# Optimization experiments

Hardware: AMD Instinct MI355X
Metric: run time of the kernel (lower is better)

Reference implementation:

```python
import jax, jax.numpy as jnp
import numpy as np

COMMITMENT_COST = 0.25


def setup_inputs() -> dict:
    key = jax.random.key(0)
    k1, k2 = jax.random.split(key)
    z = jax.random.normal(k1, (8, 256, 64, 64), dtype=jnp.float32)
    # codebook initialized uniform(-1/K, 1/K) in the original; scale a normal sample similarly
    K, D = 4096, 256
    codebook = jax.random.uniform(k2, (K, D), dtype=jnp.float32, minval=-1.0 / K, maxval=1.0 / K)
    return {"z": z, "codebook": codebook}


def reference(z, codebook):
    # z: [B, C, H, W] -> [B, H, W, C]
    B, C, H, W = z.shape
    K, D = codebook.shape  # D == C
    inputs = jnp.transpose(z, (0, 2, 3, 1))          # [B,H,W,D]
    flat = inputs.reshape(-1, D)                     # [N,D]

    d = (jnp.sum(flat ** 2, axis=1, keepdims=True)
         + jnp.sum(codebook ** 2, axis=1)
         - 2.0 * flat @ codebook.T)
    idx = jnp.argmin(d, axis=1)                      # [N]
    encodings = jax.nn.one_hot(idx, K, dtype=flat.dtype)  # [N,K]
    quantized = (encodings @ codebook).reshape(inputs.shape)  # [B,H,W,D]

    e_latent_loss = jnp.mean((jax.lax.stop_gradient(quantized) - inputs) ** 2)
    q_latent_loss = jnp.mean((quantized - jax.lax.stop_gradient(inputs)) ** 2)
    loss = q_latent_loss + COMMITMENT_COST * e_latent_loss

    # straight-through estimator
    quantized = inputs + jax.lax.stop_gradient(quantized - inputs)

    avg_probs = jnp.mean(encodings, axis=0)          # [K]
    perplexity = jnp.exp(-jnp.sum(avg_probs * jnp.log(avg_probs + 1e-10)))

    quantized_out = jnp.transpose(quantized, (0, 3, 1, 2))  # [B,C,H,W]
    return loss, quantized_out, perplexity, encodings, idx[:, None]
```

## Files before the change

### kernel.cpp

```cpp
#include <hip/hip_runtime.h>
#include <math.h>

#define N_ROWS 32768
#define K_CODES 4096
#define D_DIM 256
#define HW 4096
#define CHW 1048576

#define OFF_LOSS  0
#define OFF_QUANT 1ULL
#define OFF_PERP  8388609ULL
#define OFF_ENC   8388610ULL
#define OFF_IDX   142606338ULL

#define WS_RN   0
#define WS_EN   32768
#define WS_KEY  36864
#define WS_CNT  102400
#define WS_LOSS 106496
#define WS_CCNT 106498
#define WS_CNT2 106499
#define WS_THR  106504
#define WS_CAND 139272
#define CAP     1048576
#define WS_CBF  1187848
#define WS_NEED_BYTES ((1187848ULL + 524288ULL) * 4ULL)

#define MARGIN 1.5e-3f
#define LBUF_N 1536
#define CBUF_N 640

typedef short bf16x8 __attribute__((ext_vector_type(8)));
typedef float f32x4 __attribute__((ext_vector_type(4)));
typedef float f32x2 __attribute__((ext_vector_type(2)));

__device__ __forceinline__ unsigned short f2bf(float f) {
  unsigned u = __float_as_uint(f);
  unsigned r = u + 0x7FFFu + ((u >> 16) & 1u);
  return (unsigned short)(r >> 16);
}

__device__ __forceinline__ void async16(void* lds, const void* g) {
  typedef const __attribute__((address_space(1))) void* gvp;
  typedef __attribute__((address_space(3))) void* lvp;
  __builtin_amdgcn_global_load_lds((gvp)g, (lvp)lds, 16, 0, 0);
}

__device__ __forceinline__ float pairwise_sq_128(const float* __restrict__ p, int stride) {
  float r[8];
#pragma unroll
  for (int j = 0; j < 8; ++j) { float v = p[(size_t)j * stride]; r[j] = v * v; }
#pragma unroll
  for (int g = 1; g < 16; ++g) {
#pragma unroll
    for (int j = 0; j < 8; ++j) { float v = p[(size_t)(g * 8 + j) * stride]; r[j] += v * v; }
  }
  return ((r[0] + r[1]) + (r[2] + r[3])) + ((r[4] + r[5]) + (r[6] + r[7]));
}

__global__ void rownorm_k(const float* __restrict__ z, float* __restrict__ rn) {
  int row = blockIdx.x * 256 + threadIdx.x;
  const float* p = z + (size_t)(row >> 12) * CHW + (row & (HW - 1));
  rn[row] = pairwise_sq_128(p, HW) + pairwise_sq_128(p + (size_t)128 * HW, HW);
}

__global__ void enorm_k(const float* __restrict__ cb, float* __restrict__ en) {
  int k = blockIdx.x * 256 + threadIdx.x;
  const float* p = cb + (size_t)k * D_DIM;
  en[k] = pairwise_sq_128(p, 1) + pairwise_sq_128(p + 128, 1);
}

__global__ void cbbf_k(const float* __restrict__ cb, unsigned short* __restrict__ cbf) {
  int i = (blockIdx.x * 256 + threadIdx.x) * 4;
  float4 v = *(const float4*)(cb + i);
  unsigned d0 = f2bf(v.x) | ((unsigned)f2bf(v.y) << 16);
  unsigned d1 = f2bf(v.z) | ((unsigned)f2bf(v.w) << 16);
  *(int2*)(cbf + i) = make_int2((int)d0, (int)d1);
}

__device__ __forceinline__ void stageB(const unsigned short* __restrict__ cbf,
                                       short* bs, int tile, int ph2, int tid) {
#pragma unroll
  for (int k = 0; k < 4; ++k) {
    int i = tid + k * 256;
    int ks2 = i >> 9, s = i & 511;
    int ct = s >> 6, g = (s >> 4) & 3, m = s & 15;
    const unsigned short* src =
        cbf + (size_t)(tile * 128 + ct * 16 + m) * 256 + ph2 * 64 + ks2 * 32 + g * 8;
    async16(bs + (size_t)i * 8, src);
  }
}

__global__ __launch_bounds__(256, 2) void pass5v_k(
    const float* __restrict__ z, const float* __restrict__ cb,
    const unsigned short* __restrict__ cbf,
    const float* __restrict__ en, float* __restrict__ rn,
    float* __restrict__ enc, unsigned long long* __restrict__ key,
    unsigned int* __restrict__ cand, unsigned int* __restrict__ cnt2) {
  __shared__ __align__(16) short ASw[4 * 8 * 64 * 8];
  __shared__ __align__(16) short BS2[2 * 1024 * 8];
  __shared__ unsigned int lbuf[2 * LBUF_N];
  __shared__ unsigned int cbuf[CBUF_N];
  __shared__ float rmf[64];
  __shared__ float rn_s[64];
  __shared__ unsigned int lcnt, ccnt;

  const int tid = threadIdx.x;
  const int lane = tid & 63;
  const int w = tid >> 6;
  const int row_base = blockIdx.x * 64;
  const float* zb = z + (size_t)(row_base >> 12) * CHW + (row_base & (HW - 1));

  if (tid == 0) { lcnt = 0; ccnt = 0; }

  {
    float* pf = (float*)BS2;
    int f4 = tid & 15;
    int r0 = f4 * 4;
    int g16 = tid >> 4;
#pragma unroll
    for (int it = 0; it < 2; ++it) {
      int c_oct = (tid >> 4) + it * 16;
      float4 v[8];
#pragma unroll
      for (int j = 0; j < 8; ++j)
        v[j] = *(const float4*)(zb + (size_t)(c_oct * 8 + j) * HW + r0);
      int s = c_oct >> 2, g = c_oct & 3;
#pragma unroll
      for (int i = 0; i < 4; ++i) {
        int r = r0 + i, rt = r >> 4, m = r & 15;
        int dw[4];
#pragma unroll
        for (int k = 0; k < 4; ++k) {
          unsigned lo = f2bf(((const float*)&v[2 * k])[i]);
          unsigned hi = f2bf(((const float*)&v[2 * k + 1])[i]);
          dw[k] = (int)(lo | (hi << 16));
        }
        *(int4*)&ASw[(((rt * 8 + s) * 64) + g * 16 + m) * 8] =
            make_int4(dw[0], dw[1], dw[2], dw[3]);
#pragma unroll
        for (int j = 0; j < 8; ++j) {
          float x = ((const float*)&v[j])[i];
          pf[(g16 * 64 + r) * 8 + j] = x * x;
        }
      }
      __syncthreads();
      if (tid < 64) {
        float racc[8];
#pragma unroll
        for (int j = 0; j < 8; ++j) racc[j] = pf[(size_t)tid * 8 + j];
        for (int gg = 1; gg < 16; ++gg)
#pragma unroll
          for (int j = 0; j < 8; ++j) racc[j] += pf[(gg * 64 + tid) * 8 + j];
        float h = ((racc[0] + racc[1]) + (racc[2] + racc[3])) +
                  ((racc[4] + racc[5]) + (racc[6] + racc[7]));
        if (it == 0) rmf[tid] = h;
        else {
          float tot = rmf[tid] + h;
          rn[row_base + tid] = tot;
          rn_s[tid] = tot;
        }
      }
      __syncthreads();
    }
  }

  unsigned rowenc[4];
#pragma unroll
  for (int r = 0; r < 4; ++r)
    rowenc[r] = (unsigned)(row_base + w * 16 + (lane >> 4) * 4 + r) << 12;

  float rmin[4] = {3.4e38f, 3.4e38f, 3.4e38f, 3.4e38f};

  stageB(cbf, BS2, 0, 0, tid);
  int pidx = 0;
  for (int tile = 0; tile < 32; ++tile) {
    float ev[8];
#pragma unroll
    for (int ct = 0; ct < 8; ++ct) ev[ct] = en[tile * 128 + ct * 16 + (lane & 15)];

    f32x4 acc[8];
#pragma unroll
    for (int ct = 0; ct < 8; ++ct) acc[ct] = (f32x4){0.f, 0.f, 0.f, 0.f};

#pragma unroll
    for (int ph2 = 0; ph2 < 4; ++ph2, ++pidx) {
      __syncthreads();
      int nx = pidx + 1;
      if (nx < 128) stageB(cbf, BS2 + (nx & 1) * 8192, nx >> 2, nx & 3, tid);

      const short* bb = BS2 + (pidx & 1) * 8192;
      bf16x8 a0 = *(const bf16x8*)&ASw[((w * 8 + ph2 * 2 + 0) * 64 + lane) * 8];
      bf16x8 a1 = *(const bf16x8*)&ASw[((w * 8 + ph2 * 2 + 1) * 64 + lane) * 8];
      __builtin_amdgcn_s_setprio(1);
#pragma unroll
      for (int ct = 0; ct < 8; ++ct) {
        bf16x8 b0 = *(const bf16x8*)&bb[(ct * 64 + lane) * 8];
        acc[ct] = __builtin_amdgcn_mfma_f32_16x16x32_bf16(a0, b0, acc[ct], 0, 0, 0);
      }
#pragma unroll
      for (int ct = 0; ct < 8; ++ct) {
        bf16x8 b1 = *(const bf16x8*)&bb[(512 + ct * 64 + lane) * 8];
        acc[ct] = __builtin_amdgcn_mfma_f32_16x16x32_bf16(a1, b1, acc[ct], 0, 0, 0);
      }
      __builtin_amdgcn_s_setprio(0);
    }

    {
      f32x2 zz = (f32x2){0.f, 0.f};
      f32x2* dst = (f32x2*)enc + ((size_t)blockIdx.x * 32 + tile) * 4096 + tid;
#pragma unroll
      for (int k = 0; k < 16; ++k)
        __builtin_nontemporal_store(zz, dst + k * 256);
    }

#pragma unroll
    for (int ct = 0; ct < 8; ++ct)
#pragma unroll
      for (int r = 0; r < 4; ++r)
        rmin[r] = fminf(rmin[r], ev[ct] - 2.0f * acc[ct][r]);

    float thr2[4];
#pragma unroll
    for (int r = 0; r < 4; ++r) {
      float v = rmin[r];
      v = fminf(v, __shfl_xor(v, 1));
      v = fminf(v, __shfl_xor(v, 2));
      v = fminf(v, __shfl_xor(v, 4));
      v = fminf(v, __shfl_xor(v, 8));
      thr2[r] = v + MARGIN;
    }

#pragma unroll
    for (int ct = 0; ct < 8; ++ct) {
      unsigned code = (unsigned)(tile * 128 + ct * 16 + (lane & 15));
#pragma unroll
      for (int r = 0; r < 4; ++r) {
        float s = ev[ct] - 2.0f * acc[ct][r];
        if (s <= thr2[r]) {
          unsigned pc = rowenc[r] | code;
          unsigned pos = atomicAdd(&lcnt, 1u);
          if (pos < LBUF_N) {
            lbuf[2 * pos] = pc;
            lbuf[2 * pos + 1] = __float_as_uint(s);
          } else {
            unsigned g = atomicAdd(cnt2, 1u);
            if (g < CAP) cand[g] = pc;
          }
        }
      }
    }
  }

#pragma unroll
  for (int r = 0; r < 4; ++r) {
    float v = rmin[r];
    v = fminf(v, __shfl_xor(v, 1));
    v = fminf(v, __shfl_xor(v, 2));
    v = fminf(v, __shfl_xor(v, 4));
    v = fminf(v, __shfl_xor(v, 8));
    if ((lane & 15) == 0) rmf[(rowenc[r] >> 12) & 63] = v;
  }

  __syncthreads();
  unsigned n = lcnt; if (n > LBUF_N) n = LBUF_N;
  for (unsigned i0 = 0; i0 < n; i0 += 256) {
    unsigned i = i0 + tid;
    bool keep = false; unsigned pc = 0;
    if (i < n) {
      pc = lbuf[2 * i];
      float s = __uint_as_float(lbuf[2 * i + 1]);
      keep = (s <= rmf[(pc >> 12) & 63] + MARGIN);
    }
    unsigned long long m = __ballot(keep);
    unsigned wb = 0;
    if ((tid & 63) == 0 && m) wb = atomicAdd(&ccnt, (unsigned)__popcll(m));
    wb = __shfl(wb, 0);
    if (keep) {
      unsigned off = (unsigned)__popcll(m & ((1ull << (tid & 63)) - 1ull));
      unsigned g = wb + off;
      if (g < CBUF_N) cbuf[g] = pc;
      else { unsigned gg = atomicAdd(cnt2, 1u); if (gg < CAP) cand[gg] = pc; }
    }
  }

  __syncthreads();
  unsigned nv = ccnt; if (nv > CBUF_N) nv = CBUF_N;
  for (unsigned i = tid; i < nv; i += 256) {
    unsigned pc = cbuf[i];
    unsigned row = pc >> 12, code = pc & 4095u;
    const float* x = z + (size_t)(row >> 12) * CHW + (row & (HW - 1));
    const float* e = cb + (size_t)code * D_DIM;
    float acc = 0.0f;
#pragma unroll 8
    for (int c = 0; c < D_DIM; ++c) acc = fmaf(x[(size_t)c * HW], e[c], acc);
    float d = (rn_s[row & 63] + en[code]) - 2.0f * acc;
    unsigned long long k64 = ((unsigned long long)__float_as_uint(d) << 32) | code;
    atomicMin(&key[row], k64);
  }
}

__global__ void verify_k(const float* __restrict__ z, const float* __restrict__ cb,
                         const float* __restrict__ rn, const float* __restrict__ en,
                         const unsigned int* __restrict__ cand,
                         const unsigned int* __restrict__ cnt,
                         unsigned long long* __restrict__ key) {
  unsigned total = *cnt; if (total > CAP) total = CAP;
  for (unsigned i = blockIdx.x * 256 + threadIdx.x; i < total; i += gridDim.x * 256) {
    unsigned pc = cand[i];
    unsigned row = pc >> 12, code = pc & 4095u;
    const float* x = z + (size_t)(row >> 12) * CHW + (row & (HW - 1));
    const float* e = cb + (size_t)code * D_DIM;
    float acc = 0.0f;
#pragma unroll 8
    for (int c = 0; c < D_DIM; ++c) acc = fmaf(x[(size_t)c * HW], e[c], acc);
    float d = (rn[row] + en[code]) - 2.0f * acc;
    unsigned long long k64 = ((unsigned long long)__float_as_uint(d) << 32) | code;
    atomicMin(&key[row], k64);
  }
}

#define BM 128
#define BN 128
#define BK 32
#define KQ 1024
#define ES_S 36
__global__ __launch_bounds__(256, 3) void argmin_fb(
    const float* __restrict__ z, const float* __restrict__ cb,
    const float* __restrict__ rn, const float* __restrict__ en,
    unsigned long long* __restrict__ key, const unsigned int* __restrict__ guard) {
  if (guard && *guard <= CAP) return;
  __shared__ union {
    struct { float Xs[BK * BM]; float Es[BN * ES_S]; } s;
    struct { float rv[BM * 16]; int ri[BM * 16]; } r;
  } sh;
  const int tid = threadIdx.x;
  const int tx = tid & 15, ty = tid >> 4;
  const int row_base = (blockIdx.x >> 2) * BM;
  const int q = blockIdx.x & 3;
  const float* zb = z + (size_t)(row_base >> 12) * CHW + (row_base & (HW - 1));
  float rnv[8];
#pragma unroll
  for (int i = 0; i < 8; ++i) rnv[i] = rn[row_base + ty * 8 + i];
  float bestV[8]; int bestI[8];
#pragma unroll
  for (int i = 0; i < 8; ++i) { bestV[i] = 3.4e38f; bestI[i] = 0; }
  for (int t0 = q * KQ; t0 < q * KQ + KQ; t0 += BN) {
    float acc[8][8];
#pragma unroll
    for (int i = 0; i < 8; ++i)
#pragma unroll
      for (int j = 0; j < 8; ++j) acc[i][j] = 0.0f;
    for (int kb = 0; kb < D_DIM; kb += BK) {
      __syncthreads();
#pragma unroll
      for (int k = 0; k < 4; ++k) {
        int l4 = tid + k * 256, cl = l4 >> 5, ro = (l4 & 31) << 2;
        *(float4*)&sh.s.Xs[cl * BM + ro] = *(const float4*)(zb + (size_t)(kb + cl) * HW + ro);
      }
#pragma unroll
      for (int k = 0; k < 4; ++k) {
        int l4 = tid + k * 256, kl = l4 >> 3, cq = (l4 & 7) << 2;
        *(float4*)&sh.s.Es[kl * ES_S + cq] =
            *(const float4*)(cb + (size_t)(t0 + kl) * D_DIM + kb + cq);
      }
      __syncthreads();
#pragma unroll
      for (int c4 = 0; c4 < BK / 4; ++c4) {
        float4 ef[8];
#pragma unroll
        for (int j = 0; j < 8; ++j)
          ef[j] = *(const float4*)&sh.s.Es[(tx + 16 * j) * ES_S + c4 * 4];
#pragma unroll
        for (int cc = 0; cc < 4; ++cc) {
          int c = c4 * 4 + cc;
          float4 xa = *(const float4*)&sh.s.Xs[c * BM + ty * 8];
          float4 xb = *(const float4*)&sh.s.Xs[c * BM + ty * 8 + 4];
          float xv[8] = {xa.x, xa.y, xa.z, xa.w, xb.x, xb.y, xb.z, xb.w};
          float evv[8] = {((const float*)&ef[0])[cc], ((const float*)&ef[1])[cc],
                          ((const float*)&ef[2])[cc], ((const float*)&ef[3])[cc],
                          ((const float*)&ef[4])[cc], ((const float*)&ef[5])[cc],
                          ((const float*)&ef[6])[cc], ((const float*)&ef[7])[cc]};
#pragma unroll
          for (int i = 0; i < 8; ++i)
#pragma unroll
            for (int j = 0; j < 8; ++j) acc[i][j] = fmaf(xv[i], evv[j], acc[i][j]);
        }
      }
    }
#pragma unroll
    for (int j = 0; j < 8; ++j) {
      int code = t0 + tx + 16 * j;
      float ev = en[code];
#pragma unroll
      for (int i = 0; i < 8; ++i) {
        float d = (rnv[i] + ev) - 2.0f * acc[i][j];
        if (d < bestV[i]) { bestV[i] = d; bestI[i] = code; }
      }
    }
  }
  __syncthreads();
#pragma unroll
  for (int i = 0; i < 8; ++i) {
    sh.r.rv[(ty * 8 + i) * 16 + tx] = bestV[i];
    sh.r.ri[(ty * 8 + i) * 16 + tx] = bestI[i];
  }
  __syncthreads();
  if (tid < BM) {
    float bv = sh.r.rv[tid * 16]; int bi = sh.r.ri[tid * 16];
    for (int t = 1; t < 16; ++t) {
      float v = sh.r.rv[tid * 16 + t]; int ii = sh.r.ri[tid * 16 + t];
      if (v < bv || (v == bv && ii < bi)) { bv = v; bi = ii; }
    }
    unsigned long long k64 = ((unsigned long long)__float_as_uint(bv) << 32) | (unsigned)bi;
    atomicMin(&key[row_base + tid], k64);
  }
}

__global__ void quant2_k(const float* __restrict__ z, const float* __restrict__ cb,
                         const unsigned long long* __restrict__ key,
                         unsigned int* __restrict__ counts, float* __restrict__ out,
                         double* __restrict__ losssum) {
  __shared__ double red[256];
  int bh = blockIdx.x, b = bh >> 6, h = bh & 63;
  int tid = threadIdx.x, w = tid & 63, c0 = tid >> 6;
  int n = (b << 12) + (h << 6) + w;
  int iv = (int)(unsigned int)(key[n] & 0xffffffffULL);
  if (c0 == 0) {
    out[OFF_IDX + n] = (float)iv;
    out[OFF_ENC + (size_t)n * K_CODES + iv] = 1.0f;
    atomicAdd(&counts[iv], 1u);
  }
  const float* cbr = cb + (size_t)iv * D_DIM;
  size_t zoff = (size_t)b * CHW + (size_t)(h << 6) + w;
  double s = 0.0;
  for (int c = c0; c < D_DIM; c += 4) {
    float zv = z[zoff + (size_t)c * HW];
    float qv = cbr[c];
    float diff = qv - zv;
    out[OFF_QUANT + zoff + (size_t)c * HW] = zv + diff;
    double dd = (double)qv - (double)zv;
    s += dd * dd;
  }
  red[tid] = s;
  __syncthreads();
  for (int st = 128; st > 0; st >>= 1) {
    if (tid < st) red[tid] += red[tid + st];
    __syncthreads();
  }
  if (tid == 0) atomicAdd(losssum, red[0]);
}

__global__ void final_k(const unsigned int* __restrict__ counts,
                        const double* __restrict__ losssum, float* __restrict__ out) {
  __shared__ double red[256];
  int tid = threadIdx.x;
  double s = 0.0;
  for (int k = tid; k < K_CODES; k += 256) {
    double p = (double)counts[k] / 32768.0;
    s += p * log(p + 1e-10);
  }
  red[tid] = s;
  __syncthreads();
  for (int st = 128; st > 0; st >>= 1) {
    if (tid < st) red[tid] += red[tid + st];
    __syncthreads();
  }
  if (tid == 0) {
    out[OFF_PERP] = (float)exp(-red[0]);
    out[OFF_LOSS] = (float)(1.25 * losssum[0] / 8388608.0);
  }
}

extern "C" void kernel_launch(void* const* d_in, const int* in_sizes, int n_in,
                              void* d_out, int out_size, void* d_ws, size_t ws_size,
                              hipStream_t stream) {
  (void)in_sizes; (void)n_in; (void)out_size;
  const float* z = (const float*)d_in[0];
  const float* cb = (const float*)d_in[1];
  float* out = (float*)d_out;
  float* ws = (float*)d_ws;

  float* rn = ws + WS_RN;
  float* en = ws + WS_EN;
  unsigned long long* key = (unsigned long long*)(ws + WS_KEY);
  unsigned int* counts = (unsigned int*)(ws + WS_CNT);
  double* losssum = (double*)(ws + WS_LOSS);

  hipMemsetAsync(ws + WS_KEY, 0xFF, (size_t)N_ROWS * sizeof(unsigned long long), stream);

  enorm_k<<<K_CODES / 256, 256, 0, stream>>>(cb, en);

  if (ws_size >= WS_NEED_BYTES) {
    unsigned int* cnt2 = (unsigned int*)(ws + WS_CNT2);
    unsigned int* cand = (unsigned int*)(ws + WS_CAND);
    unsigned short* cbf = (unsigned short*)(ws + WS_CBF);
    hipMemsetAsync(ws + WS_CNT, 0, (WS_THR - WS_CNT) * sizeof(float), stream);
    cbbf_k<<<(K_CODES * D_DIM / 4) / 256, 256, 0, stream>>>(cb, cbf);
    pass5v_k<<<N_ROWS / 64, 256, 0, stream>>>(z, cb, cbf, en, rn,
                                              out + OFF_ENC, key, cand, cnt2);
    verify_k<<<256, 256, 0, stream>>>(z, cb, rn, en, cand, cnt2, key);
    argmin_fb<<<(N_ROWS / BM) * 4, 256, 0, stream>>>(z, cb, rn, en, key, cnt2);
  } else {
    hipMemsetAsync(out + OFF_ENC, 0, (size_t)N_ROWS * K_CODES * sizeof(float), stream);
    rownorm_k<<<N_ROWS / 256, 256, 0, stream>>>(z, rn);
    hipMemsetAsync(ws + WS_CNT, 0, K_CODES * sizeof(unsigned int) + 2 * sizeof(double), stream);
    argmin_fb<<<(N_ROWS / BM) * 4, 256, 0, stream>>>(z, cb, rn, en, key, nullptr);
  }

  quant2_k<<<512, 256, 0, stream>>>(z, cb, key, counts, out, losssum);
  final_k<<<1, 256, 0, stream>>>(counts, losssum, out);
}
```

Measured before the change: 760.2 us.

## Fuse quantize/loss epilogue into candidate-search kernel when no overflow

Each block of the fused search kernel tracks a per-row minimum in shared memory. When its local buffers did not overflow, it writes the index, one-hot entry, quantized output, code counts and loss partial directly, then sets a per-block flag. The later quant2 kernel returns early for flagged blocks. This removes a second pass over z and the codebook rows and the reload of keys, at the cost of more epilogue work and registers inside the heavy kernel. Correctness relies on the block-local minimum matching the global result, which holds only when no candidates spilled to the global verify path.

```diff
diff --git a/kernel.cpp b/kernel.cpp
--- a/kernel.cpp
+++ b/kernel.cpp
@@ -91,18 +91,21 @@
   }
 }
 
-__global__ __launch_bounds__(256, 2) void pass5v_k(
+__global__ __launch_bounds__(256, 2) void pass6q_k(
     const float* __restrict__ z, const float* __restrict__ cb,
     const unsigned short* __restrict__ cbf,
     const float* __restrict__ en, float* __restrict__ rn,
-    float* __restrict__ enc, unsigned long long* __restrict__ key,
-    unsigned int* __restrict__ cand, unsigned int* __restrict__ cnt2) {
+    float* __restrict__ out, unsigned long long* __restrict__ key,
+    unsigned int* __restrict__ cand, unsigned int* __restrict__ cnt2,
+    unsigned int* __restrict__ counts, double* __restrict__ losssum,
+    unsigned int* __restrict__ flags) {
   __shared__ __align__(16) short ASw[4 * 8 * 64 * 8];
   __shared__ __align__(16) short BS2[2 * 1024 * 8];
-  __shared__ unsigned int lbuf[2 * LBUF_N];
+  __shared__ __align__(16) unsigned int lbuf[2 * LBUF_N];
   __shared__ unsigned int cbuf[CBUF_N];
   __shared__ float rmf[64];
   __shared__ float rn_s[64];
+  __shared__ unsigned long long kmin[64];
   __shared__ unsigned int lcnt, ccnt;
 
   const int tid = threadIdx.x;
@@ -110,6 +113,7 @@
   const int w = tid >> 6;
   const int row_base = blockIdx.x * 64;
   const float* zb = z + (size_t)(row_base >> 12) * CHW + (row_base & (HW - 1));
+  float* enc = out + OFF_ENC;
 
   if (tid == 0) { lcnt = 0; ccnt = 0; }
 
@@ -261,6 +265,7 @@
     v = fminf(v, __shfl_xor(v, 8));
     if ((lane & 15) == 0) rmf[(rowenc[r] >> 12) & 63] = v;
   }
+  if (tid < 64) kmin[tid] = 0xFFFFFFFFFFFFFFFFULL;
 
   __syncthreads();
   unsigned n = lcnt; if (n > LBUF_N) n = LBUF_N;
@@ -296,7 +301,40 @@
     for (int c = 0; c < D_DIM; ++c) acc = fmaf(x[(size_t)c * HW], e[c], acc);
     float d = (rn_s[row & 63] + en[code]) - 2.0f * acc;
     unsigned long long k64 = ((unsigned long long)__float_as_uint(d) << 32) | code;
+    atomicMin(&kmin[row & 63], k64);
     atomicMin(&key[row], k64);
+  }
+
+  __syncthreads();
+  bool ok = (lcnt <= LBUF_N) && (ccnt <= CBUF_N);
+  if (ok) {
+    double* red = (double*)lbuf;
+    int rloc = tid & 63, c0 = tid >> 6;
+    int row = row_base + rloc;
+    int iv = (int)(unsigned int)(kmin[rloc] & 0xffffffffULL);
+    if (c0 == 0) {
+      out[OFF_IDX + row] = (float)iv;
+      out[OFF_ENC + (size_t)row * K_CODES + iv] = 1.0f;
+      atomicAdd(&counts[iv], 1u);
+    }
+    const float* cbr = cb + (size_t)iv * D_DIM;
+    size_t zoff = (size_t)(row >> 12) * CHW + (row & (HW - 1));
+    double s = 0.0;
+    for (int c = c0; c < D_DIM; c += 4) {
+      float zv = z[zoff + (size_t)c * HW];
+      float qv = cbr[c];
+      float diff = qv - zv;
+      out[OFF_QUANT + zoff + (size_t)c * HW] = zv + diff;
+      double dd = (double)qv - (double)zv;
+      s += dd * dd;
+    }
+    red[tid] = s;
+    __syncthreads();
+    for (int st = 128; st > 0; st >>= 1) {
+      if (tid < st) red[tid] += red[tid + st];
+      __syncthreads();
+    }
+    if (tid == 0) { atomicAdd(losssum, red[0]); flags[blockIdx.x] = 1u; }
   }
 }
 
@@ -419,8 +457,10 @@
 
 __global__ void quant2_k(const float* __restrict__ z, const float* __restrict__ cb,
                          const unsigned long long* __restrict__ key,
+                         const unsigned int* __restrict__ flags,
                          unsigned int* __restrict__ counts, float* __restrict__ out,
                          double* __restrict__ losssum) {
+  if (flags && flags[blockIdx.x]) return;
   __shared__ double red[256];
   int bh = blockIdx.x, b = bh >> 6, h = bh & 63;
   int tid = threadIdx.x, w = tid & 63, c0 = tid >> 6;
@@ -493,21 +533,23 @@
 
   if (ws_size >= WS_NEED_BYTES) {
     unsigned int* cnt2 = (unsigned int*)(ws + WS_CNT2);
+    unsigned int* flags = (unsigned int*)(ws + WS_THR);
     unsigned int* cand = (unsigned int*)(ws + WS_CAND);
     unsigned short* cbf = (unsigned short*)(ws + WS_CBF);
-    hipMemsetAsync(ws + WS_CNT, 0, (WS_THR - WS_CNT) * sizeof(float), stream);
+    hipMemsetAsync(ws + WS_CNT, 0, (WS_THR - WS_CNT + 512) * sizeof(float), stream);
     cbbf_k<<<(K_CODES * D_DIM / 4) / 256, 256, 0, stream>>>(cb, cbf);
-    pass5v_k<<<N_ROWS / 64, 256, 0, stream>>>(z, cb, cbf, en, rn,
-                                              out + OFF_ENC, key, cand, cnt2);
+    pass6q_k<<<N_ROWS / 64, 256, 0, stream>>>(z, cb, cbf, en, rn, out, key,
+                                              cand, cnt2, counts, losssum, flags);
     verify_k<<<256, 256, 0, stream>>>(z, cb, rn, en, cand, cnt2, key);
     argmin_fb<<<(N_ROWS / BM) * 4, 256, 0, stream>>>(z, cb, rn, en, key, cnt2);
+    quant2_k<<<512, 256, 0, stream>>>(z, cb, key, flags, counts, out, losssum);
   } else {
     hipMemsetAsync(out + OFF_ENC, 0, (size_t)N_ROWS * K_CODES * sizeof(float), stream);
     rownorm_k<<<N_ROWS / 256, 256, 0, stream>>>(z, rn);
     hipMemsetAsync(ws + WS_CNT, 0, K_CODES * sizeof(unsigned int) + 2 * sizeof(double), stream);
     argmin_fb<<<(N_ROWS / BM) * 4, 256, 0, stream>>>(z, cb, rn, en, key, nullptr);
-  }
-
-  quant2_k<<<512, 256, 0, stream>>>(z, cb, key, counts, out, losssum);
+    quant2_k<<<512, 256, 0, stream>>>(z, cb, key, nullptr, counts, out, losssum);
+  }
+
   final_k<<<1, 256, 0, stream>>>(counts, losssum, out);
 }
```

Result: no change. 762.5 us (+0.3%).
